# Kernel optimization log

Measured on AMD Instinct MI355X. Metric: run time of the kernel, lower is better.

## Reference

```python
import jax, jax.numpy as jnp
import numpy as np

B, NCLASS, ATTN, CH = 256, 1000, 32, 512
P = 0.5  # exchange probability threshold


def setup_inputs() -> dict:
    key = jax.random.key(0)
    k1, k2, k3, k4 = jax.random.split(key, 4)
    features = jax.random.normal(k1, (B, ATTN, CH), dtype=jnp.float32)
    idx = jax.random.randint(k2, (B,), 0, NCLASS)
    labels = jax.nn.one_hot(idx, NCLASS, dtype=jnp.float32)  # one-hot class labels
    anchor = jax.random.normal(k3, (NCLASS, ATTN, CH), dtype=jnp.float32)
    cache = jnp.zeros((NCLASS, ATTN, CH), dtype=jnp.float32)
    count = jnp.zeros((NCLASS,), dtype=jnp.float32)
    rand_u = jax.random.uniform(k4, (B, ATTN), dtype=jnp.float32)  # replaces torch.rand in forward
    return {"features": features, "labels": labels, "anchor": anchor,
            "cache": cache, "count": count, "rand_u": rand_u}


def reference(features, labels, anchor, cache, count, rand_u):
    # label-weighted outer-product accumulate: (B,A,C) x (B,N) -> (N,A,C)
    # (torch materializes (B,N,A,C) via broadcast; this is the fused contraction)
    batch_cache = jnp.einsum('bac,bn->nac', features, labels)
    new_cache = cache + batch_cache
    new_count = count + labels.sum(axis=0)
    # exchange: random per-(sample, attention-part) blend with class anchor
    mask = (rand_u > P).astype(features.dtype)[:, :, None]  # (B,A,1)
    cls = jnp.argmax(labels, axis=1)                         # (B,)
    exch_features = mask * anchor[cls] + (1.0 - mask) * features
    return exch_features, new_cache, new_count
```

## Files before the change

### kernel.cpp

```cpp
#include <hip/hip_runtime.h>

constexpr int kB  = 256;
constexpr int kN  = 1000;
constexpr int kA  = 32;
constexpr int kC  = 512;
constexpr int kAC = kA * kC;
constexpr int kFeat  = kB * kAC;
constexpr int kCache = kN * kAC;

__global__ __launch_bounds__(256) void k_prep(
    const float* __restrict__ labels,
    int*   __restrict__ cls)
{
    const int wave = threadIdx.x >> 6;
    const int lane = threadIdx.x & 63;
    const int b = blockIdx.x * 4 + wave;
    const float* row = labels + (size_t)b * kN;
    float best = -3.4e38f;
    int   bidx = kN;
    for (int n = lane; n < kN; n += 64) {
        float v = row[n];
        if (v > best) { best = v; bidx = n; }
    }
    #pragma unroll
    for (int off = 32; off >= 1; off >>= 1) {
        float ov = __shfl_xor(best, off, 64);
        int   oi = __shfl_xor(bidx, off, 64);
        if (ov > best || (ov == best && oi < bidx)) { best = ov; bidx = oi; }
    }
    if (lane == 0) cls[b] = bidx;
}

__global__ __launch_bounds__(256) void k_main(
    const float* __restrict__ features,
    const float* __restrict__ anchor,
    const float* __restrict__ cache,
    const float* __restrict__ count,
    const float* __restrict__ rand_u,
    const int*   __restrict__ cls,
    float* __restrict__ out_feat,
    float* __restrict__ out_cache,
    float* __restrict__ out_count)
{
    const int blk = blockIdx.x;
    if (blk < kN) {
        const int n = blk;
        const int t = threadIdx.x;

        __shared__ unsigned long long masks[4];
        const int myc = cls[t];
        unsigned long long mb = __ballot(myc == n);
        if ((t & 63) == 0) masks[t >> 6] = mb;

        const float4* src = (const float4*)(cache + (size_t)n * kAC);
        float4*       dst = (float4*)(out_cache + (size_t)n * kAC);
        float4 acc[16];
        #pragma unroll
        for (int i = 0; i < 16; ++i) acc[i] = src[t + i * 256];

        __syncthreads();

        int mtot = 0;
        #pragma unroll
        for (int w = 0; w < 4; ++w) {
            unsigned long long m = masks[w];
            mtot += __popcll(m);
            while (m) {
                const int bit = __ffsll((long long)m) - 1;
                m &= m - 1;
                const int b = w * 64 + bit;
                const float4* f = (const float4*)(features + (size_t)b * kAC);
                #pragma unroll
                for (int i = 0; i < 16; ++i) {
                    float4 v = f[t + i * 256];
                    acc[i].x += v.x; acc[i].y += v.y;
                    acc[i].z += v.z; acc[i].w += v.w;
                }
            }
        }
        #pragma unroll
        for (int i = 0; i < 16; ++i) dst[t + i * 256] = acc[i];

        if (t == 0) out_count[n] = count[n] + (float)mtot;
    } else {
        const int rblk = blk - kN;
        const int row  = rblk * 2 + (threadIdx.x >> 7);
        const int c4   = threadIdx.x & 127;
        const int b    = row >> 5;
        const int a    = row & 31;

        const float ru = rand_u[row];
        const float4* src = (ru > 0.5f)
            ? (const float4*)(anchor + ((size_t)cls[b] * kA + a) * kC)
            : (const float4*)(features + (size_t)row * kC);
        ((float4*)(out_feat + (size_t)row * kC))[c4] = src[c4];
    }
}

extern "C" void kernel_launch(void* const* d_in, const int* in_sizes, int n_in,
                              void* d_out, int out_size, void* d_ws, size_t ws_size,
                              hipStream_t stream) {
    const float* features = (const float*)d_in[0];
    const float* labels   = (const float*)d_in[1];
    const float* anchor   = (const float*)d_in[2];
    const float* cache    = (const float*)d_in[3];
    const float* count    = (const float*)d_in[4];
    const float* rand_u   = (const float*)d_in[5];

    float* out_feat  = (float*)d_out;
    float* out_cache = out_feat + kFeat;
    float* out_count = out_cache + kCache;

    int* cls = (int*)d_ws;

    k_prep<<<kB / 4, 256, 0, stream>>>(labels, cls);
    k_main<<<kN + (kB * kA) / 2, 256, 0, stream>>>(features, anchor, cache, count,
                                                   rand_u, cls,
                                                   out_feat, out_cache, out_count);
}
```

Before: 204.2 us.

## Split cache blocks in halves, precompute exchange source rows, use nontemporal memory ops

Each class's cache slice is now handled by two blocks instead of one, doubling block count and cutting per-thread accumulator registers. k_prep precomputes a tagged source-row index per (sample, attention) row, so the exchange path no longer reads rand_u and cls itself. Exchange blocks now cover 8 rows each. Cache loads and all output stores use nontemporal builtins to avoid polluting cache with streaming data. The mask ballot is duplicated across the two halves, and the extra index indirection adds a dependent load.

```diff
diff --git a/kernel.cpp b/kernel.cpp
--- a/kernel.cpp
+++ b/kernel.cpp
@@ -1,4 +1,6 @@
 #include <hip/hip_runtime.h>
+
+typedef float f32x4 __attribute__((ext_vector_type(4)));
 
 constexpr int kB  = 256;
 constexpr int kN  = 1000;
@@ -7,10 +9,23 @@
 constexpr int kAC = kA * kC;
 constexpr int kFeat  = kB * kAC;
 constexpr int kCache = kN * kAC;
+constexpr int kRows  = kB * kA;
+
+constexpr int kCacheSplit = 2;
+constexpr int kCacheBlks  = kN * kCacheSplit;
+constexpr int kF4PerClass = kAC / 4;
+constexpr int kF4PerHalf  = kF4PerClass / kCacheSplit;
+constexpr int kAccN       = kF4PerHalf / 256;
+
+constexpr int kExRowsPerBlk = 8;
+constexpr int kExBlks = kRows / kExRowsPerBlk;
+constexpr int kExIters = kExRowsPerBlk * 128 / 256;
 
 __global__ __launch_bounds__(256) void k_prep(
     const float* __restrict__ labels,
-    int*   __restrict__ cls)
+    const float* __restrict__ rand_u,
+    int* __restrict__ cls,
+    int* __restrict__ srcrow)
 {
     const int wave = threadIdx.x >> 6;
     const int lane = threadIdx.x & 63;
@@ -29,6 +44,12 @@
         if (ov > best || (ov == best && oi < bidx)) { best = ov; bidx = oi; }
     }
     if (lane == 0) cls[b] = bidx;
+    if (lane < kA) {
+        const int r = b * kA + lane;
+        const float ru = rand_u[r];
+        srcrow[r] = (ru > 0.5f) ? (int)(0x80000000u | (unsigned)(bidx * kA + lane))
+                                : r;
+    }
 }
 
 __global__ __launch_bounds__(256) void k_main(
@@ -36,27 +57,30 @@
     const float* __restrict__ anchor,
     const float* __restrict__ cache,
     const float* __restrict__ count,
-    const float* __restrict__ rand_u,
     const int*   __restrict__ cls,
+    const int*   __restrict__ srcrow,
     float* __restrict__ out_feat,
     float* __restrict__ out_cache,
     float* __restrict__ out_count)
 {
     const int blk = blockIdx.x;
-    if (blk < kN) {
-        const int n = blk;
-        const int t = threadIdx.x;
+    const int t = threadIdx.x;
+    if (blk < kCacheBlks) {
+        const int n    = blk >> 1;
+        const int half = blk & 1;
 
         __shared__ unsigned long long masks[4];
         const int myc = cls[t];
         unsigned long long mb = __ballot(myc == n);
         if ((t & 63) == 0) masks[t >> 6] = mb;
 
-        const float4* src = (const float4*)(cache + (size_t)n * kAC);
-        float4*       dst = (float4*)(out_cache + (size_t)n * kAC);
-        float4 acc[16];
+        const size_t base = (size_t)n * kF4PerClass + (size_t)half * kF4PerHalf;
+        const f32x4* src = (const f32x4*)cache + base;
+        f32x4*       dst = (f32x4*)out_cache + base;
+        f32x4 acc[kAccN];
         #pragma unroll
-        for (int i = 0; i < 16; ++i) acc[i] = src[t + i * 256];
+        for (int i = 0; i < kAccN; ++i)
+            acc[i] = __builtin_nontemporal_load(&src[t + i * 256]);
 
         __syncthreads();
 
@@ -69,31 +93,35 @@
                 const int bit = __ffsll((long long)m) - 1;
                 m &= m - 1;
                 const int b = w * 64 + bit;
-                const float4* f = (const float4*)(features + (size_t)b * kAC);
+                const f32x4* f = (const f32x4*)features
+                                + (size_t)b * kF4PerClass + (size_t)half * kF4PerHalf;
                 #pragma unroll
-                for (int i = 0; i < 16; ++i) {
-                    float4 v = f[t + i * 256];
-                    acc[i].x += v.x; acc[i].y += v.y;
-                    acc[i].z += v.z; acc[i].w += v.w;
-                }
+                for (int i = 0; i < kAccN; ++i)
+                    acc[i] += f[t + i * 256];
             }
         }
         #pragma unroll
-        for (int i = 0; i < 16; ++i) dst[t + i * 256] = acc[i];
+        for (int i = 0; i < kAccN; ++i)
+            __builtin_nontemporal_store(acc[i], &dst[t + i * 256]);
 
-        if (t == 0) out_count[n] = count[n] + (float)mtot;
+        if (t == 0 && half == 0) out_count[n] = count[n] + (float)mtot;
     } else {
-        const int rblk = blk - kN;
-        const int row  = rblk * 2 + (threadIdx.x >> 7);
-        const int c4   = threadIdx.x & 127;
-        const int b    = row >> 5;
-        const int a    = row & 31;
-
-        const float ru = rand_u[row];
-        const float4* src = (ru > 0.5f)
-            ? (const float4*)(anchor + ((size_t)cls[b] * kA + a) * kC)
-            : (const float4*)(features + (size_t)row * kC);
-        ((float4*)(out_feat + (size_t)row * kC))[c4] = src[c4];
+        const int rblk = blk - kCacheBlks;
+        const int j0   = rblk * (kExRowsPerBlk * 128);
+        const f32x4* features4 = (const f32x4*)features;
+        const f32x4* anchor4   = (const f32x4*)anchor;
+        f32x4*       out4      = (f32x4*)out_feat;
+        #pragma unroll
+        for (int k = 0; k < kExIters; ++k) {
+            const int j   = j0 + k * 256 + t;
+            const int row = j >> 7;
+            const int c4  = j & 127;
+            const int s   = srcrow[row];
+            const f32x4* srcb = (s >= 0) ? features4 : anchor4;
+            const int r = s & 0x7fffffff;
+            f32x4 v = srcb[(size_t)r * 128 + c4];
+            __builtin_nontemporal_store(v, &out4[j]);
+        }
     }
 }
 
@@ -111,10 +139,11 @@
     float* out_cache = out_feat + kFeat;
     float* out_count = out_cache + kCache;
 
-    int* cls = (int*)d_ws;
+    int* cls    = (int*)d_ws;
+    int* srcrow = cls + kB;
 
-    k_prep<<<kB / 4, 256, 0, stream>>>(labels, cls);
-    k_main<<<kN + (kB * kA) / 2, 256, 0, stream>>>(features, anchor, cache, count,
-                                                   rand_u, cls,
-                                                   out_feat, out_cache, out_count);
+    k_prep<<<kB / 4, 256, 0, stream>>>(labels, rand_u, cls, srcrow);
+    k_main<<<kCacheBlks + kExBlks, 256, 0, stream>>>(features, anchor, cache, count,
+                                                     cls, srcrow,
+                                                     out_feat, out_cache, out_count);
 }
```

Result: faster. 196.9 us (-3.6%).
